# Optimization experiments

Hardware: AMD Instinct MI355X
Metric: run time of the kernel (lower is better)

Reference implementation:

```python
import jax, jax.numpy as jnp
import numpy as np

NUM_HEADS = 16
WINDOW_SIZE = 256  # config.window_size; layer is 'local'


def setup_inputs() -> dict:
    key = jax.random.key(0)
    ks = jax.random.split(key, 8)
    B, S, H = 4, 2048, 1024
    scale = 1.0 / np.sqrt(H)
    return {
        "x": jax.random.normal(ks[0], (B, S, H), dtype=jnp.float32),
        "x_clean": jax.random.normal(ks[1], (B, S, H), dtype=jnp.float32),
        "ablation_mask": jax.random.uniform(ks[2], (B, S, H), dtype=jnp.float32),
        "Wq": jax.random.normal(ks[3], (H, H), dtype=jnp.float32) * scale,
        "Wk": jax.random.normal(ks[4], (H, H), dtype=jnp.float32) * scale,
        "Wv": jax.random.normal(ks[5], (H, H), dtype=jnp.float32) * scale,
        "Wo": jax.random.normal(ks[6], (H, H), dtype=jnp.float32) * scale,
        "bo": jnp.zeros((H,), dtype=jnp.float32),
    }


def reference(x, x_clean, ablation_mask, Wq, Wk, Wv, Wo, bo):
    B, S, H = x.shape
    nh, hd = NUM_HEADS, H // NUM_HEADS

    def proj(inp, W):  # torch Linear: inp @ W.T -> split heads -> [B, nh, S, hd]
        return jnp.einsum('bsh,oh->bso', inp, W).reshape(B, S, nh, hd).transpose(0, 2, 1, 3)

    q = proj(x, Wq)
    k = proj(x_clean, Wk)
    v = proj(x_clean, Wv)

    # NOTE: original applies NO 1/sqrt(head_dim) scaling.
    scores = jnp.einsum('bnsd,bntd->bnst', q, k)  # [B, nh, S, S]

    i = jnp.arange(S)[:, None]
    j = jnp.arange(S)[None, :]
    # local mask: forbid future (j > i) OR too-far past (j <= i - window)
    masked = (j > i) | (j <= i - WINDOW_SIZE)
    scores = jnp.where(masked[None, None, :, :], -jnp.inf, scores)

    attn = jax.nn.softmax(scores, axis=-1)
    context = jnp.einsum('bnst,bntd->bnsd', attn, v)          # [B, nh, S, hd]
    context = context.transpose(0, 2, 1, 3).reshape(B, S, H)   # merge heads
    context = context * ablation_mask
    return jnp.einsum('bsh,oh->bso', context, Wo) + bo
```

## Files before the change

### kernel.cpp

```cpp
#include <hip/hip_runtime.h>
#include <hip/hip_bf16.h>
#include <cstddef>

#define SB 4
#define SS 2048
#define SH 1024
#define NH 16
#define HD 64
#define WIN 256

typedef __attribute__((ext_vector_type(8))) short bf16x8;
typedef __attribute__((ext_vector_type(8))) _Float16 f16x8;
typedef __attribute__((ext_vector_type(2))) __fp16 fp16v2;
typedef __attribute__((ext_vector_type(4))) float f32x4;

static __device__ __forceinline__ ushort2 pk_bf16(float a, float b) {
    __hip_bfloat162 h = __float22bfloat162_rn(make_float2(a, b));
    union { __hip_bfloat162 h2; ushort2 u2; } u;
    u.h2 = h;
    return u.u2;
}
static __device__ __forceinline__ unsigned short pk1(float a) {
    return pk_bf16(a, 0.f).x;
}

static __device__ __forceinline__ void async16(const void* gptr, void* lptr) {
    __builtin_amdgcn_global_load_lds(
        (const __attribute__((address_space(1))) unsigned int*)gptr,
        (__attribute__((address_space(3))) unsigned int*)lptr, 16, 0, 0);
}

__global__ __launch_bounds__(256) void cvt_all(
    const float* __restrict__ x,  const float* __restrict__ xc,
    const float* __restrict__ Wq, const float* __restrict__ Wk,
    const float* __restrict__ Wv, const float* __restrict__ Wo,
    _Float16* __restrict__ xh,  _Float16* __restrict__ xch,
    _Float16* __restrict__ Wqh, _Float16* __restrict__ Wkh,
    _Float16* __restrict__ Wvh, _Float16* __restrict__ Woh)
{
    const int I4 = SB * SS * SH / 4;
    const int W4 = SH * SH / 4;
    int idx = blockIdx.x * 256 + threadIdx.x;
    const float* src;
    _Float16* dst;
    int off;
    if (idx < I4) { src = x; dst = xh; off = idx; }
    else if (idx < 2 * I4) { src = xc; dst = xch; off = idx - I4; }
    else {
        int r = idx - 2 * I4;
        int wi = r >> 18;
        off = r & (W4 - 1);
        src = (wi == 0) ? Wq : (wi == 1) ? Wk : (wi == 2) ? Wv : Wo;
        dst = (wi == 0) ? Wqh : (wi == 1) ? Wkh : (wi == 2) ? Wvh : Woh;
    }
    float4 v = ((const float4*)src)[off];
    union { fp16v2 h[2]; uint2 u; } t;
    t.h[0] = __builtin_amdgcn_cvt_pkrtz(v.x, v.y);
    t.h[1] = __builtin_amdgcn_cvt_pkrtz(v.z, v.w);
    ((uint2*)dst)[off] = t.u;
}

__global__ __launch_bounds__(256) void gemm_qkv(
    const _Float16* __restrict__ xh, const _Float16* __restrict__ xch,
    const _Float16* __restrict__ Wqh, const _Float16* __restrict__ Wkh,
    const _Float16* __restrict__ Wvh,
    _Float16* __restrict__ Qh, _Float16* __restrict__ Kh,
    unsigned short* __restrict__ Vt)
{
    const int M = SB * SS, N = SH, K = SH;
    __shared__ __align__(16) unsigned short smem[128 * 136];
    _Float16* Ah = (_Float16*)smem;
    _Float16* Bh = (_Float16*)smem + 8192;

    const int z = blockIdx.z;
    const _Float16* A = (z == 0) ? xh : xch;
    const _Float16* W = (z == 0) ? Wqh : (z == 1) ? Wkh : Wvh;

    const int tid = threadIdx.x;
    const int m0 = blockIdx.x * 128;
    const int n0 = blockIdx.y * 128;
    const int wave = tid >> 6;
    const int lane = tid & 63;
    const int wm = (wave & 1) * 64;
    const int wn = (wave >> 1) * 64;
    const int lrow = lane & 15;
    const int lk8 = (lane >> 4) * 8;
    const int rq = (lane >> 4) * 4;

    f32x4 acc[4][4];
#pragma unroll
    for (int i = 0; i < 4; ++i)
#pragma unroll
        for (int j = 0; j < 4; ++j)
            acc[i][j] = (f32x4){0.f, 0.f, 0.f, 0.f};

    for (int k0 = 0; k0 < K; k0 += 64) {
        __syncthreads();
#pragma unroll
        for (int ki = 0; ki < 2; ++ki)
#pragma unroll
            for (int u = 0; u < 2; ++u) {
                int reg = u * 4 + wave;
                int slot = reg * 64 + lane;
                int row = slot >> 2;
                int k8 = (slot & 3) * 8;
                async16(A + (size_t)(m0 + row) * K + k0 + ki * 32 + k8,
                        Ah + ki * 4096 + reg * 512);
                async16(W + (size_t)(n0 + row) * K + k0 + ki * 32 + k8,
                        Bh + ki * 4096 + reg * 512);
            }
        __syncthreads();

#pragma unroll
        for (int ki = 0; ki < 2; ++ki) {
            f16x8 bf[4];
#pragma unroll
            for (int j = 0; j < 4; ++j)
                bf[j] = *(const f16x8*)&Bh[ki * 4096 + (wn + j * 16 + lrow) * 32 + lk8];
#pragma unroll
            for (int i = 0; i < 4; ++i) {
                f16x8 af = *(const f16x8*)&Ah[ki * 4096 + (wm + i * 16 + lrow) * 32 + lk8];
#pragma unroll
                for (int j = 0; j < 4; ++j)
                    acc[i][j] = __builtin_amdgcn_mfma_f32_16x16x32_f16(af, bf[j], acc[i][j], 0, 0, 0);
            }
        }
    }

    if (z < 2) {
        _Float16* C = (z == 0) ? Qh : Kh;
        _Float16* T = (_Float16*)smem;
        __syncthreads();
#pragma unroll
        for (int i = 0; i < 4; ++i) {
            int rloc = wm + i * 16 + rq;
#pragma unroll
            for (int j = 0; j < 4; ++j) {
                int cl = wn + j * 16 + lrow;
#pragma unroll
                for (int r = 0; r < 4; ++r)
                    T[(rloc + r) * 136 + cl] = (_Float16)acc[i][j][r];
            }
        }
        __syncthreads();
#pragma unroll
        for (int u = 0; u < 8; ++u) {
            int slot = u * 256 + tid;
            int row = slot >> 4;
            int c8 = (slot & 15) * 8;
            *(uint4*)(C + (size_t)(m0 + row) * N + n0 + c8) =
                *(const uint4*)&T[row * 136 + c8];
        }
    } else {
        unsigned short* T = smem;
#pragma unroll
        for (int p = 0; p < 2; ++p) {
            __syncthreads();
            if (wn == p * 64) {
#pragma unroll
                for (int i = 0; i < 4; ++i) {
                    int mloc = wm + i * 16 + rq;
#pragma unroll
                    for (int j = 0; j < 4; ++j) {
                        int cl = j * 16 + lrow;
                        *(ushort4*)&T[cl * 136 + mloc] = make_ushort4(
                            pk1(acc[i][j][0]), pk1(acc[i][j][1]),
                            pk1(acc[i][j][2]), pk1(acc[i][j][3]));
                    }
                }
            }
            __syncthreads();
#pragma unroll
            for (int u = 0; u < 4; ++u) {
                int slot = u * 256 + tid;
                int cl = slot >> 4;
                int m8 = (slot & 15) * 8;
                *(uint4*)(Vt + (size_t)(n0 + p * 64 + cl) * M + m0 + m8) =
                    *(const uint4*)&T[cl * 136 + m8];
            }
        }
    }
}

__global__ __launch_bounds__(256) void gemm_o(
    const _Float16* __restrict__ A, const _Float16* __restrict__ W,
    const float* __restrict__ bias, float* __restrict__ C)
{
    const int M = SB * SS, N = SH, K = SH;
    __shared__ __align__(16) unsigned short smem[2 * 128 * 64];
    _Float16* Ah = (_Float16*)smem;
    _Float16* Bh = (_Float16*)smem + 8192;

    const int tid = threadIdx.x;
    const int m0 = blockIdx.x * 128;
    const int n0 = blockIdx.y * 128;
    const int wave = tid >> 6;
    const int lane = tid & 63;
    const int wm = (wave & 1) * 64;
    const int wn = (wave >> 1) * 64;
    const int lrow = lane & 15;
    const int lk8 = (lane >> 4) * 8;
    const int rq = (lane >> 4) * 4;

    f32x4 acc[4][4];
#pragma unroll
    for (int i = 0; i < 4; ++i)
#pragma unroll
        for (int j = 0; j < 4; ++j)
            acc[i][j] = (f32x4){0.f, 0.f, 0.f, 0.f};

    for (int k0 = 0; k0 < K; k0 += 64) {
        __syncthreads();
#pragma unroll
        for (int ki = 0; ki < 2; ++ki)
#pragma unroll
            for (int u = 0; u < 2; ++u) {
                int reg = u * 4 + wave;
                int slot = reg * 64 + lane;
                int row = slot >> 2;
                int k8 = (slot & 3) * 8;
                async16(A + (size_t)(m0 + row) * K + k0 + ki * 32 + k8,
                        Ah + ki * 4096 + reg * 512);
                async16(W + (size_t)(n0 + row) * K + k0 + ki * 32 + k8,
                        Bh + ki * 4096 + reg * 512);
            }
        __syncthreads();

#pragma unroll
        for (int ki = 0; ki < 2; ++ki) {
            f16x8 bf[4];
#pragma unroll
            for (int j = 0; j < 4; ++j)
                bf[j] = *(const f16x8*)&Bh[ki * 4096 + (wn + j * 16 + lrow) * 32 + lk8];
#pragma unroll
            for (int i = 0; i < 4; ++i) {
                f16x8 af = *(const f16x8*)&Ah[ki * 4096 + (wm + i * 16 + lrow) * 32 + lk8];
#pragma unroll
                for (int j = 0; j < 4; ++j)
                    acc[i][j] = __builtin_amdgcn_mfma_f32_16x16x32_f16(af, bf[j], acc[i][j], 0, 0, 0);
            }
        }
    }

#pragma unroll
    for (int i = 0; i < 4; ++i) {
        int rbase = m0 + wm + i * 16 + rq;
#pragma unroll
        for (int j = 0; j < 4; ++j) {
            int col = n0 + wn + j * 16 + lrow;
            float badd = bias[col];
#pragma unroll
            for (int r = 0; r < 4; ++r)
                C[(size_t)(rbase + r) * N + col] = acc[i][j][r] + badd;
        }
    }
}

__global__ __launch_bounds__(512, 4) void attn5(
    const _Float16* Qg, const _Float16* __restrict__ Kg,
    const unsigned short* __restrict__ Vtg, const float* __restrict__ amask,
    _Float16* ctxg)
{
    __shared__ __align__(16) _Float16 K_s[2][2 * 64 * 32];
    __shared__ __align__(16) unsigned short V_s[2][2 * 64 * 32];
    __shared__ __align__(16) unsigned short P_s[8][32 * 72];

    const int t = threadIdx.x;
    const int wave = t >> 6, lane = t & 63;
    const int id = blockIdx.x;
    const int qb = id >> 6;
    const int pr = id & 63;
    const int h = pr & 15, b = pr >> 4;
    const int t0 = qb * 256;
    const int wq = t0 + wave * 32;
    const int lrow = lane & 15;
    const int lk8 = (lane >> 4) * 8;
    const int rq = (lane >> 4) * 4;
    const int M = SB * SS;
    unsigned short* P = P_s[wave];

    const int ski = t >> 8;
    const int srow = (t & 255) >> 2;
    const int se8 = (t & 3) * 8;

    f16x8 qf[2][2];
#pragma unroll
    for (int i = 0; i < 2; ++i)
#pragma unroll
        for (int ki = 0; ki < 2; ++ki)
            qf[i][ki] = *(const f16x8*)(Qg +
                (size_t)(b * SS + wq + i * 16 + lrow) * SH + h * HD + ki * 32 + lk8);

    f32x4 o[2][4];
    float lsum[2][4];
#pragma unroll
    for (int i = 0; i < 2; ++i)
#pragma unroll
        for (int j = 0; j < 4; ++j) o[i][j] = (f32x4){0.f, 0.f, 0.f, 0.f};
#pragma unroll
    for (int i = 0; i < 2; ++i)
#pragma unroll
        for (int r = 0; r < 4; ++r) lsum[i][r] = 0.f;

    int cl0 = t0 - (WIN - 1);
    cl0 = cl0 < 0 ? 0 : cl0;
    const int c_lo = cl0 >> 6;
    const int c_hi = (t0 >> 6) + 3;

    auto stage = [&](int c, int buf) {
        const int key0 = c * 64;
        async16(Kg + (size_t)(b * SS + key0 + srow) * SH + h * HD + ski * 32 + se8,
                (_Float16*)K_s[buf] + wave * 512);
        async16(Vtg + (size_t)(h * HD + srow) * M + b * SS + key0 + ski * 32 + se8,
                (unsigned short*)V_s[buf] + wave * 512);
    };

    stage(c_lo, c_lo & 1);
    __syncthreads();

    for (int c = c_lo; c <= c_hi; ++c) {
        const int cur = c & 1;
        if (c < c_hi) stage(c + 1, cur ^ 1);
        const int key0 = c * 64;
        if (key0 <= wq + 31 && key0 + 63 >= wq - (WIN - 1)) {
            const _Float16* Kc = (const _Float16*)K_s[cur];
            const unsigned short* Vc = (const unsigned short*)V_s[cur];

            f32x4 s[2][4];
#pragma unroll
            for (int i = 0; i < 2; ++i)
#pragma unroll
                for (int j = 0; j < 4; ++j) s[i][j] = (f32x4){0.f, 0.f, 0.f, 0.f};
#pragma unroll
            for (int ki = 0; ki < 2; ++ki)
#pragma unroll
                for (int j = 0; j < 4; ++j) {
                    f16x8 bh = *(const f16x8*)&Kc[ki * 2048 + (j * 16 + lrow) * 32 + lk8];
#pragma unroll
                    for (int i = 0; i < 2; ++i)
                        s[i][j] = __builtin_amdgcn_mfma_f32_16x16x32_f16(qf[i][ki], bh, s[i][j], 0, 0, 0);
                }

#pragma unroll
            for (int i = 0; i < 2; ++i)
#pragma unroll
                for (int j = 0; j < 4; ++j) {
                    int jg = key0 + j * 16 + lrow;
#pragma unroll
                    for (int r = 0; r < 4; ++r) {
                        int qg = wq + i * 16 + rq + r;
                        float p = (jg <= qg && jg > qg - WIN) ? __expf(s[i][j][r]) : 0.f;
                        lsum[i][r] += p;
                        P[(i * 16 + rq + r) * 72 + j * 16 + lrow] = pk1(p);
                    }
                }

#pragma unroll
            for (int ki = 0; ki < 2; ++ki) {
                bf16x8 pf[2];
#pragma unroll
                for (int i = 0; i < 2; ++i)
                    pf[i] = *(const bf16x8*)&P[(i * 16 + lrow) * 72 + ki * 32 + lk8];
#pragma unroll
                for (int j = 0; j < 4; ++j) {
                    bf16x8 vf = *(const bf16x8*)&Vc[ki * 2048 + (j * 16 + lrow) * 32 + lk8];
#pragma unroll
                    for (int i = 0; i < 2; ++i)
                        o[i][j] = __builtin_amdgcn_mfma_f32_16x16x32_bf16(pf[i], vf, o[i][j], 0, 0, 0);
                }
            }
        }
        __syncthreads();
    }

#pragma unroll
    for (int i = 0; i < 2; ++i)
#pragma unroll
        for (int r = 0; r < 4; ++r) {
#pragma unroll
            for (int m = 1; m < 16; m <<= 1)
                lsum[i][r] += __shfl_xor(lsum[i][r], m);
        }

    _Float16* Pf = (_Float16*)P;
#pragma unroll
    for (int i = 0; i < 2; ++i)
#pragma unroll
        for (int r = 0; r < 4; ++r) {
            float inv = 1.f / lsum[i][r];
#pragma unroll
            for (int j = 0; j < 4; ++j)
                Pf[(i * 16 + rq + r) * 72 + j * 16 + lrow] = (_Float16)(o[i][j][r] * inv);
        }
#pragma unroll
    for (int u = 0; u < 4; ++u) {
        int slot = u * 64 + lane;
        int ro = slot >> 3;
        int d8 = (slot & 7) * 8;
        f16x8 v = *(const f16x8*)&Pf[ro * 72 + d8];
        size_t g = (size_t)(b * SS + wq + ro) * SH + h * HD + d8;
        float4 ma = *(const float4*)(amask + g);
        float4 mb = *(const float4*)(amask + g + 4);
        f16x8 rs;
        rs[0] = (_Float16)((float)v[0] * ma.x);
        rs[1] = (_Float16)((float)v[1] * ma.y);
        rs[2] = (_Float16)((float)v[2] * ma.z);
        rs[3] = (_Float16)((float)v[3] * ma.w);
        rs[4] = (_Float16)((float)v[4] * mb.x);
        rs[5] = (_Float16)((float)v[5] * mb.y);
        rs[6] = (_Float16)((float)v[6] * mb.z);
        rs[7] = (_Float16)((float)v[7] * mb.w);
        *(f16x8*)(ctxg + g) = rs;
    }
}

extern "C" void kernel_launch(void* const* d_in, const int* in_sizes, int n_in,
                              void* d_out, int out_size, void* d_ws, size_t ws_size,
                              hipStream_t stream)
{
    const float* x     = (const float*)d_in[0];
    const float* xc    = (const float*)d_in[1];
    const float* amask = (const float*)d_in[2];
    const float* Wq    = (const float*)d_in[3];
    const float* Wk    = (const float*)d_in[4];
    const float* Wv    = (const float*)d_in[5];
    const float* Wo    = (const float*)d_in[6];
    const float* bo    = (const float*)d_in[7];
    float* out = (float*)d_out;

    const int M = SB * SS;
    const size_t BUF = (size_t)M * SH;
    const size_t WBUF = (size_t)SH * SH;
    _Float16* xh  = (_Float16*)d_ws;
    _Float16* xch = xh + BUF;
    _Float16* Qh  = xch + BUF;
    _Float16* Kh  = Qh + BUF;
    unsigned short* Vt = (unsigned short*)(Kh + BUF);
    _Float16* Wqh = (_Float16*)(Vt + BUF);
    _Float16* Wkh = Wqh + WBUF;
    _Float16* Wvh = Wkh + WBUF;
    _Float16* Woh = Wvh + WBUF;
    _Float16* ctx = Qh;

    const int total4 = 2 * (M * SH / 4) + 4 * (SH * SH / 4);
    hipLaunchKernelGGL(cvt_all, dim3(total4 / 256), dim3(256), 0, stream,
                       x, xc, Wq, Wk, Wv, Wo, xh, xch, Wqh, Wkh, Wvh, Woh);

    hipLaunchKernelGGL(gemm_qkv, dim3(M / 128, SH / 128, 3), dim3(256), 0, stream,
                       xh, xch, Wqh, Wkh, Wvh, Qh, Kh, Vt);

    hipLaunchKernelGGL(attn5, dim3((SS / 256) * NH * SB), dim3(512), 0, stream,
                       Qh, Kh, Vt, amask, ctx);

    hipLaunchKernelGGL(gemm_o, dim3(M / 128, SH / 128), dim3(256), 0, stream,
                       ctx, Woh, bo, out);
}
```

Before: 281.9 us.

## Rewrite projection GEMMs as 8-wave double-buffered pipelined 128x256 tile kernels

Replaces both the QKV and output projection GEMMs with a shared core that uses 512-thread blocks and 128x256 tiles. It double-buffers K-tiles in LDS with async global-to-LDS loads issued between MFMA phases, XOR-swizzles the LDS layout to avoid bank conflicts, and raises wave priority around the MFMA bursts. The aim is to hide global load latency and the per-iteration barrier stalls of the old load-then-compute loop. The cost is more LDS per block, many more fine-grained barriers, and hand-placed waitcnt counters that must match the number of outstanding loads.

After: 271.1 us. -3.8%, faster.

```diff
diff --git a/kernel.cpp b/kernel.cpp
--- a/kernel.cpp
+++ b/kernel.cpp
@@ -29,6 +29,8 @@
         (const __attribute__((address_space(1))) unsigned int*)gptr,
         (__attribute__((address_space(3))) unsigned int*)lptr, 16, 0, 0);
 }
+
+#define CFENCE() asm volatile("" ::: "memory")
 
 __global__ __launch_bounds__(256) void cvt_all(
     const float* __restrict__ x,  const float* __restrict__ xc,
@@ -60,32 +62,159 @@
     ((uint2*)dst)[off] = t.u;
 }
 
-__global__ __launch_bounds__(256) void gemm_qkv(
+static __device__ __forceinline__ void gemm8_core(
+    const _Float16* __restrict__ A, const _Float16* __restrict__ W,
+    int m0, int n0, unsigned short* __restrict__ smem, f32x4 (&acc)[4][4])
+{
+    const int K = SH;
+    const int NT = K / 64;
+    const int tid = threadIdx.x;
+    const int w = tid >> 6, lane = tid & 63;
+    const int wm = (w >> 2) * 64;
+    const int wn = (w & 3) * 64;
+    const int lrow = lane & 15;
+    const int lk8 = (lane >> 4) * 8;
+    const int swz = (lrow & 4) << 2;
+
+    const int srow = w * 8 + (lane >> 3);
+    const int scol = ((lane & 7) << 3) ^ (((lane >> 3) & 4) << 2);
+    const _Float16* aS = A + (size_t)(m0 + srow) * K + scol;
+    const _Float16* bS = W + (size_t)(n0 + srow) * K + scol;
+
+    auto stA = [&](int tile, int half) {
+        async16(aS + (size_t)(half * 64) * K + tile * 64,
+                smem + ((tile & 1) << 13) + half * 4096 + w * 512);
+    };
+    auto stB = [&](int tile, int half) {
+        async16(bS + (size_t)(half * 128) * K + tile * 64,
+                smem + 16384 + ((tile & 1) << 14) + half * 8192 + w * 512);
+        async16(bS + (size_t)(half * 128 + 64) * K + tile * 64,
+                smem + 16384 + ((tile & 1) << 14) + half * 8192 + 4096 + w * 512);
+    };
+
+    f16x8 a[2][2];
+    f16x8 b[2][2][2];
+
+    stA(0, 0); stA(0, 1);
+    stB(0, 0); stB(0, 1);
+    stB(1, 0); stB(1, 1);
+    asm volatile("s_waitcnt vmcnt(4)" ::: "memory");
+    __builtin_amdgcn_s_barrier();
+    CFENCE();
+
+    for (int t = 0; t < NT; ++t) {
+        const int cur = t & 1;
+        unsigned short* LA = smem + (cur << 13);
+        unsigned short* LB = smem + 16384 + (cur << 14);
+
+#pragma unroll
+        for (int m = 0; m < 2; ++m)
+#pragma unroll
+            for (int ks = 0; ks < 2; ++ks)
+                a[m][ks] = *(const f16x8*)(LA + (wm + m * 16 + lrow) * 64 + ((ks * 32 + lk8) ^ swz));
+#pragma unroll
+        for (int n = 0; n < 2; ++n)
+#pragma unroll
+            for (int ks = 0; ks < 2; ++ks)
+                b[0][n][ks] = *(const f16x8*)(LB + (wn + n * 16 + lrow) * 64 + ((ks * 32 + lk8) ^ swz));
+        if (t + 1 < NT) stA(t + 1, 0);
+        CFENCE();
+        __builtin_amdgcn_s_barrier();
+        CFENCE();
+        asm volatile("s_waitcnt lgkmcnt(0)" ::: "memory");
+        __builtin_amdgcn_s_setprio(1);
+#pragma unroll
+        for (int ks = 0; ks < 2; ++ks)
+#pragma unroll
+            for (int m = 0; m < 2; ++m)
+#pragma unroll
+                for (int n = 0; n < 2; ++n)
+                    acc[m][n] = __builtin_amdgcn_mfma_f32_16x16x32_f16(a[m][ks], b[0][n][ks], acc[m][n], 0, 0, 0);
+        __builtin_amdgcn_s_setprio(0);
+        CFENCE();
+        __builtin_amdgcn_s_barrier();
+        CFENCE();
+
+#pragma unroll
+        for (int n = 0; n < 2; ++n)
+#pragma unroll
+            for (int ks = 0; ks < 2; ++ks)
+                b[1][n][ks] = *(const f16x8*)(LB + (wn + 32 + n * 16 + lrow) * 64 + ((ks * 32 + lk8) ^ swz));
+        if (t + 1 < NT) stA(t + 1, 1);
+        CFENCE();
+        __builtin_amdgcn_s_barrier();
+        CFENCE();
+        asm volatile("s_waitcnt lgkmcnt(0)" ::: "memory");
+        __builtin_amdgcn_s_setprio(1);
+#pragma unroll
+        for (int ks = 0; ks < 2; ++ks)
+#pragma unroll
+            for (int m = 0; m < 2; ++m)
+#pragma unroll
+                for (int n = 0; n < 2; ++n)
+                    acc[m][2 + n] = __builtin_amdgcn_mfma_f32_16x16x32_f16(a[m][ks], b[1][n][ks], acc[m][2 + n], 0, 0, 0);
+        __builtin_amdgcn_s_setprio(0);
+        CFENCE();
+        __builtin_amdgcn_s_barrier();
+        CFENCE();
+
+#pragma unroll
+        for (int m = 0; m < 2; ++m)
+#pragma unroll
+            for (int ks = 0; ks < 2; ++ks)
+                a[m][ks] = *(const f16x8*)(LA + (wm + 32 + m * 16 + lrow) * 64 + ((ks * 32 + lk8) ^ swz));
+        if (t + 2 < NT) stB(t + 2, 0);
+        CFENCE();
+        __builtin_amdgcn_s_barrier();
+        CFENCE();
+        asm volatile("s_waitcnt lgkmcnt(0)" ::: "memory");
+        __builtin_amdgcn_s_setprio(1);
+#pragma unroll
+        for (int ks = 0; ks < 2; ++ks)
+#pragma unroll
+            for (int m = 0; m < 2; ++m)
+#pragma unroll
+                for (int n = 0; n < 2; ++n)
+                    acc[2 + m][2 + n] = __builtin_amdgcn_mfma_f32_16x16x32_f16(a[m][ks], b[1][n][ks], acc[2 + m][2 + n], 0, 0, 0);
+        __builtin_amdgcn_s_setprio(0);
+        CFENCE();
+        __builtin_amdgcn_s_barrier();
+        CFENCE();
+
+        if (t + 2 < NT) stB(t + 2, 1);
+        CFENCE();
+        __builtin_amdgcn_s_barrier();
+        CFENCE();
+        __builtin_amdgcn_s_setprio(1);
+#pragma unroll
+        for (int ks = 0; ks < 2; ++ks)
+#pragma unroll
+            for (int m = 0; m < 2; ++m)
+#pragma unroll
+                for (int n = 0; n < 2; ++n)
+                    acc[2 + m][n] = __builtin_amdgcn_mfma_f32_16x16x32_f16(a[m][ks], b[0][n][ks], acc[2 + m][n], 0, 0, 0);
+        __builtin_amdgcn_s_setprio(0);
+        if (t < NT - 2) asm volatile("s_waitcnt vmcnt(4)" ::: "memory");
+        else            asm volatile("s_waitcnt vmcnt(0)" ::: "memory");
+        __builtin_amdgcn_s_barrier();
+        CFENCE();
+    }
+    CFENCE();
+}
+
+__global__ __launch_bounds__(512, 2) void gemm_qkv8(
     const _Float16* __restrict__ xh, const _Float16* __restrict__ xch,
     const _Float16* __restrict__ Wqh, const _Float16* __restrict__ Wkh,
     const _Float16* __restrict__ Wvh,
     _Float16* __restrict__ Qh, _Float16* __restrict__ Kh,
     unsigned short* __restrict__ Vt)
 {
-    const int M = SB * SS, N = SH, K = SH;
-    __shared__ __align__(16) unsigned short smem[128 * 136];
-    _Float16* Ah = (_Float16*)smem;
-    _Float16* Bh = (_Float16*)smem + 8192;
-
+    __shared__ __align__(16) unsigned short smem[49152];
     const int z = blockIdx.z;
     const _Float16* A = (z == 0) ? xh : xch;
     const _Float16* W = (z == 0) ? Wqh : (z == 1) ? Wkh : Wvh;
-
-    const int tid = threadIdx.x;
     const int m0 = blockIdx.x * 128;
-    const int n0 = blockIdx.y * 128;
-    const int wave = tid >> 6;
-    const int lane = tid & 63;
-    const int wm = (wave & 1) * 64;
-    const int wn = (wave >> 1) * 64;
-    const int lrow = lane & 15;
-    const int lk8 = (lane >> 4) * 8;
-    const int rq = (lane >> 4) * 4;
+    const int n0 = blockIdx.y * 256;
 
     f32x4 acc[4][4];
 #pragma unroll
@@ -94,113 +223,64 @@
         for (int j = 0; j < 4; ++j)
             acc[i][j] = (f32x4){0.f, 0.f, 0.f, 0.f};
 
-    for (int k0 = 0; k0 < K; k0 += 64) {
-        __syncthreads();
-#pragma unroll
-        for (int ki = 0; ki < 2; ++ki)
-#pragma unroll
-            for (int u = 0; u < 2; ++u) {
-                int reg = u * 4 + wave;
-                int slot = reg * 64 + lane;
-                int row = slot >> 2;
-                int k8 = (slot & 3) * 8;
-                async16(A + (size_t)(m0 + row) * K + k0 + ki * 32 + k8,
-                        Ah + ki * 4096 + reg * 512);
-                async16(W + (size_t)(n0 + row) * K + k0 + ki * 32 + k8,
-                        Bh + ki * 4096 + reg * 512);
-            }
-        __syncthreads();
-
-#pragma unroll
-        for (int ki = 0; ki < 2; ++ki) {
-            f16x8 bf[4];
-#pragma unroll
-            for (int j = 0; j < 4; ++j)
-                bf[j] = *(const f16x8*)&Bh[ki * 4096 + (wn + j * 16 + lrow) * 32 + lk8];
-#pragma unroll
-            for (int i = 0; i < 4; ++i) {
-                f16x8 af = *(const f16x8*)&Ah[ki * 4096 + (wm + i * 16 + lrow) * 32 + lk8];
-#pragma unroll
-                for (int j = 0; j < 4; ++j)
-                    acc[i][j] = __builtin_amdgcn_mfma_f32_16x16x32_f16(af, bf[j], acc[i][j], 0, 0, 0);
-            }
-        }
-    }
+    gemm8_core(A, W, m0, n0, smem, acc);
+
+    const int tid = threadIdx.x;
+    const int w = tid >> 6, lane = tid & 63;
+    const int wm = (w >> 2) * 64, wn = (w & 3) * 64;
+    const int lrow = lane & 15;
+    const int rq = (lane >> 4) * 4;
+    const int M = SB * SS, N = SH;
 
     if (z < 2) {
         _Float16* C = (z == 0) ? Qh : Kh;
         _Float16* T = (_Float16*)smem;
+#pragma unroll
+        for (int m = 0; m < 4; ++m)
+#pragma unroll
+            for (int n = 0; n < 4; ++n)
+#pragma unroll
+                for (int r = 0; r < 4; ++r)
+                    T[(wm + m * 16 + rq + r) * 264 + wn + n * 16 + lrow] = (_Float16)acc[m][n][r];
         __syncthreads();
 #pragma unroll
-        for (int i = 0; i < 4; ++i) {
-            int rloc = wm + i * 16 + rq;
-#pragma unroll
-            for (int j = 0; j < 4; ++j) {
-                int cl = wn + j * 16 + lrow;
-#pragma unroll
-                for (int r = 0; r < 4; ++r)
-                    T[(rloc + r) * 136 + cl] = (_Float16)acc[i][j][r];
-            }
-        }
-        __syncthreads();
-#pragma unroll
         for (int u = 0; u < 8; ++u) {
-            int slot = u * 256 + tid;
-            int row = slot >> 4;
-            int c8 = (slot & 15) * 8;
+            int slot = u * 512 + tid;
+            int row = slot >> 5;
+            int c8 = (slot & 31) * 8;
             *(uint4*)(C + (size_t)(m0 + row) * N + n0 + c8) =
-                *(const uint4*)&T[row * 136 + c8];
+                *(const uint4*)&T[row * 264 + c8];
         }
     } else {
         unsigned short* T = smem;
 #pragma unroll
-        for (int p = 0; p < 2; ++p) {
-            __syncthreads();
-            if (wn == p * 64) {
-#pragma unroll
-                for (int i = 0; i < 4; ++i) {
-                    int mloc = wm + i * 16 + rq;
-#pragma unroll
-                    for (int j = 0; j < 4; ++j) {
-                        int cl = j * 16 + lrow;
-                        *(ushort4*)&T[cl * 136 + mloc] = make_ushort4(
-                            pk1(acc[i][j][0]), pk1(acc[i][j][1]),
-                            pk1(acc[i][j][2]), pk1(acc[i][j][3]));
-                    }
-                }
+        for (int n = 0; n < 4; ++n)
+#pragma unroll
+            for (int m = 0; m < 4; ++m) {
+                int rt = wn + n * 16 + lrow;
+                *(ushort4*)&T[rt * 136 + wm + m * 16 + rq] = make_ushort4(
+                    pk1(acc[m][n][0]), pk1(acc[m][n][1]),
+                    pk1(acc[m][n][2]), pk1(acc[m][n][3]));
             }
-            __syncthreads();
-#pragma unroll
-            for (int u = 0; u < 4; ++u) {
-                int slot = u * 256 + tid;
-                int cl = slot >> 4;
-                int m8 = (slot & 15) * 8;
-                *(uint4*)(Vt + (size_t)(n0 + p * 64 + cl) * M + m0 + m8) =
-                    *(const uint4*)&T[cl * 136 + m8];
-            }
+        __syncthreads();
+#pragma unroll
+        for (int u = 0; u < 8; ++u) {
+            int slot = u * 512 + tid;
+            int row = slot >> 4;
+            int m8 = (slot & 15) * 8;
+            *(uint4*)(Vt + (size_t)(n0 + row) * M + m0 + m8) =
+                *(const uint4*)&T[row * 136 + m8];
         }
     }
 }
 
-__global__ __launch_bounds__(256) void gemm_o(
+__global__ __launch_bounds__(512, 2) void gemm_o8(
     const _Float16* __restrict__ A, const _Float16* __restrict__ W,
     const float* __restrict__ bias, float* __restrict__ C)
 {
-    const int M = SB * SS, N = SH, K = SH;
-    __shared__ __align__(16) unsigned short smem[2 * 128 * 64];
-    _Float16* Ah = (_Float16*)smem;
-    _Float16* Bh = (_Float16*)smem + 8192;
-
-    const int tid = threadIdx.x;
+    __shared__ __align__(16) unsigned short smem[49152];
     const int m0 = blockIdx.x * 128;
-    const int n0 = blockIdx.y * 128;
-    const int wave = tid >> 6;
-    const int lane = tid & 63;
-    const int wm = (wave & 1) * 64;
-    const int wn = (wave >> 1) * 64;
-    const int lrow = lane & 15;
-    const int lk8 = (lane >> 4) * 8;
-    const int rq = (lane >> 4) * 4;
+    const int n0 = blockIdx.y * 256;
 
     f32x4 acc[4][4];
 #pragma unroll
@@ -209,49 +289,25 @@
         for (int j = 0; j < 4; ++j)
             acc[i][j] = (f32x4){0.f, 0.f, 0.f, 0.f};
 
-    for (int k0 = 0; k0 < K; k0 += 64) {
-        __syncthreads();
-#pragma unroll
-        for (int ki = 0; ki < 2; ++ki)
-#pragma unroll
-            for (int u = 0; u < 2; ++u) {
-                int reg = u * 4 + wave;
-                int slot = reg * 64 + lane;
-                int row = slot >> 2;
-                int k8 = (slot & 3) * 8;
-                async16(A + (size_t)(m0 + row) * K + k0 + ki * 32 + k8,
-                        Ah + ki * 4096 + reg * 512);
-                async16(W + (size_t)(n0 + row) * K + k0 + ki * 32 + k8,
-                        Bh + ki * 4096 + reg * 512);
-            }
-        __syncthreads();
-
-#pragma unroll
-        for (int ki = 0; ki < 2; ++ki) {
-            f16x8 bf[4];
-#pragma unroll
-            for (int j = 0; j < 4; ++j)
-                bf[j] = *(const f16x8*)&Bh[ki * 4096 + (wn + j * 16 + lrow) * 32 + lk8];
-#pragma unroll
-            for (int i = 0; i < 4; ++i) {
-                f16x8 af = *(const f16x8*)&Ah[ki * 4096 + (wm + i * 16 + lrow) * 32 + lk8];
-#pragma unroll
-                for (int j = 0; j < 4; ++j)
-                    acc[i][j] = __builtin_amdgcn_mfma_f32_16x16x32_f16(af, bf[j], acc[i][j], 0, 0, 0);
-            }
-        }
-    }
-
-#pragma unroll
-    for (int i = 0; i < 4; ++i) {
-        int rbase = m0 + wm + i * 16 + rq;
-#pragma unroll
-        for (int j = 0; j < 4; ++j) {
-            int col = n0 + wn + j * 16 + lrow;
+    gemm8_core(A, W, m0, n0, smem, acc);
+
+    const int tid = threadIdx.x;
+    const int w = tid >> 6, lane = tid & 63;
+    const int wm = (w >> 2) * 64, wn = (w & 3) * 64;
+    const int lrow = lane & 15;
+    const int rq = (lane >> 4) * 4;
+    const int N = SH;
+
+#pragma unroll
+    for (int m = 0; m < 4; ++m) {
+        int rbase = m0 + wm + m * 16 + rq;
+#pragma unroll
+        for (int n = 0; n < 4; ++n) {
+            int col = n0 + wn + n * 16 + lrow;
             float badd = bias[col];
 #pragma unroll
             for (int r = 0; r < 4; ++r)
-                C[(size_t)(rbase + r) * N + col] = acc[i][j][r] + badd;
+                C[(size_t)(rbase + r) * N + col] = acc[m][n][r] + badd;
         }
     }
 }
@@ -446,12 +502,12 @@
     hipLaunchKernelGGL(cvt_all, dim3(total4 / 256), dim3(256), 0, stream,
                        x, xc, Wq, Wk, Wv, Wo, xh, xch, Wqh, Wkh, Wvh, Woh);
 
-    hipLaunchKernelGGL(gemm_qkv, dim3(M / 128, SH / 128, 3), dim3(256), 0, stream,
+    hipLaunchKernelGGL(gemm_qkv8, dim3(M / 128, SH / 256, 3), dim3(512), 0, stream,
                        xh, xch, Wqh, Wkh, Wvh, Qh, Kh, Vt);
 
     hipLaunchKernelGGL(attn5, dim3((SS / 256) * NH * SB), dim3(512), 0, stream,
                        Qh, Kh, Vt, amask, ctx);
 
-    hipLaunchKernelGGL(gemm_o, dim3(M / 128, SH / 128), dim3(256), 0, stream,
+    hipLaunchKernelGGL(gemm_o8, dim3(M / 128, SH / 256), dim3(512), 0, stream,
                        ctx, Woh, bo, out);
 }
```
